# Kernel optimization log

Hardware: AMD Instinct MI355X
Metric: run time of the kernel (lower is better)

## Reference

```python
import jax, jax.numpy as jnp
import numpy as np

H = 2048           # hidden size
IN_F = 64          # in_features
OUT_F = 3          # out_features
NEG_SLOPE = 0.01   # LeakyReLU default


def setup_inputs() -> dict:
    key = jax.random.key(0)
    ks = jax.random.split(key, 11)
    N = 32768
    return {
        "p": jax.random.normal(ks[0], (N, IN_F), dtype=jnp.float32),
        "init_w": jax.random.normal(ks[1], (H, IN_F), dtype=jnp.float32) * 0.05,
        "init_b": jax.random.normal(ks[2], (H,), dtype=jnp.float32) * 0.05,
        "w1": jax.random.normal(ks[3], (H, H), dtype=jnp.float32) * 0.02,
        "b1": jax.random.normal(ks[4], (H,), dtype=jnp.float32) * 0.02,
        "w2": jax.random.normal(ks[5], (H, H), dtype=jnp.float32) * 0.02,
        "b2": jax.random.normal(ks[6], (H,), dtype=jnp.float32) * 0.02,
        "w3": jax.random.normal(ks[7], (H, H), dtype=jnp.float32) * 0.02,
        "b3": jax.random.normal(ks[8], (H,), dtype=jnp.float32) * 0.02,
        "out_w": jax.random.normal(ks[9], (OUT_F, H), dtype=jnp.float32) * 0.05,
        "out_b": jax.random.normal(ks[10], (OUT_F,), dtype=jnp.float32) * 0.05,
    }


def _leaky_relu(x):
    return jnp.where(x > 0, x, NEG_SLOPE * x)


def reference(p, init_w, init_b, w1, b1, w2, b2, w3, b3, out_w, out_b):
    # eval mode: StructuredDropout with eval_size=None -> plain init linear
    flat = p.reshape(-1, p.shape[-1])                      # [N, IN_F]
    x = flat @ init_w.T + init_b                           # [N, H]
    # upper-triangular mask (in==out, backflow=0 -> diagonal=0)
    mask = jnp.triu(jnp.ones((H, H), dtype=bool))
    # hidden TriangleLinear layers; flip = (i % 2 == 1)
    for W, b, flip in ((w1, b1, False), (w2, b2, True), (w3, b3, False)):
        y = _leaky_relu(x) @ jnp.where(mask, W, 0.0).T + b  # [N, H]
        x = y[..., ::-1] if flip else y
    x = _leaky_relu(x)
    out = x @ out_w.T + out_b                              # [N, OUT_F]
    return out.reshape(p.shape[:-1] + (OUT_F,))
```

## Files before the change

kernel.cpp:

```cpp
#include <hip/hip_runtime.h>
#include <hip/hip_bf16.h>

#define NEG 0.01f

using f32x4  = __attribute__((ext_vector_type(4))) float;
using bf16x8 = __attribute__((ext_vector_type(8))) short;

__device__ __forceinline__ unsigned short f2b(float f) {
  union { float f; unsigned int u; } v; v.f = f;
  unsigned int r = (v.u + 0x7fffu + ((v.u >> 16) & 1u)) >> 16;
  return (unsigned short)r;
}
__device__ __forceinline__ float b2f(unsigned int bits) {
  union { unsigned int u; float f; } v; v.u = bits << 16;
  return v.f;
}

__device__ __forceinline__ void gload16(const unsigned short* g, unsigned short* l) {
  __builtin_amdgcn_global_load_lds(
      (const __attribute__((address_space(1))) unsigned int*)g,
      (__attribute__((address_space(3))) unsigned int*)l, 16, 0, 0);
}

__global__ void k_cvt(const float* __restrict__ in, unsigned short* __restrict__ out, int n4) {
  int i = blockIdx.x * blockDim.x + threadIdx.x;
  int stride = gridDim.x * blockDim.x;
  for (; i < n4; i += stride) {
    float4 v = reinterpret_cast<const float4*>(in)[i];
    ushort4 o;
    o.x = f2b(v.x); o.y = f2b(v.y); o.z = f2b(v.z); o.w = f2b(v.w);
    reinterpret_cast<ushort4*>(out)[i] = o;
  }
}

__global__ void k_cvt_tri(const float* __restrict__ W, unsigned short* __restrict__ out, int anti) {
  const int H = 2048;
  int i = blockIdx.x;
  const float* wr = W + (size_t)i * H;
  unsigned short* orow = out + (size_t)i * H;
  if (!anti) {
    for (int j = threadIdx.x; j < H; j += blockDim.x) {
      float v = (j >= i) ? wr[j] : 0.f;
      orow[j] = f2b(v);
    }
  } else {
    for (int k = threadIdx.x; k < H; k += blockDim.x) {
      int j = H - 1 - k;
      float v = (j >= i) ? wr[j] : 0.f;
      orow[k] = f2b(v);
    }
  }
}

__launch_bounds__(512, 2)
__global__ void k_gemm8(const unsigned short* __restrict__ A, int lda,
                        const unsigned short* __restrict__ B, int ldb,
                        const float* __restrict__ bias,
                        unsigned short* __restrict__ C, int ldc,
                        int K, int mode, int NB) {
  extern __shared__ unsigned short lds[];
  const int tid = threadIdx.x;
  const int w   = tid >> 6;
  const int l   = tid & 63;

  const int G = gridDim.x;
  const int P = blockIdx.x;
  const int b = (P & 7) * (G >> 3) + (P >> 3);

  const int srow  = l >> 2;
  const int sperm = ((l & 3) - ((l >> 3) & 3)) & 3;
  const int rdoff = (l & 15) * 64 + ((((l >> 4) + ((l >> 1) & 7)) & 3) << 4);
  const int wm = w >> 2, wn = w & 3;
  const int AbaseW = wm * 16384;
  const int BbaseW = 32768 + (wn >> 1) * 16384 + (wn & 1) * 8192;

  const int npairs = NB * 4;
#pragma unroll 1
  for (int p = b; p < npairs; p += G) {
    const int by = p >> 2;
    const int pr = p & 3;
#pragma unroll 1
    for (int side = 0; side < 2; side++) {
      const int bx = side ? (7 - pr) : pr;
      const int brow = by * 256;
      const int bcol = bx * 256;
      int kstart = 0, kend = K;
      if (mode == 1) kstart = bcol;
      else if (mode == 2) kend = K - bcol;
      const int nt = (kend - kstart) >> 6;

      const unsigned short* Asrc = A + (size_t)(brow + w * 16 + srow) * lda + sperm * 8;
      const unsigned short* Bsrc = B + (size_t)(bcol + w * 16 + srow) * ldb + sperm * 8;

      auto stage_tile = [&](int tk, int bb) {
        const int kc = kstart + (tk << 6);
#pragma unroll
        for (int half = 0; half < 2; half++) {
#pragma unroll
          for (int qq = 0; qq < 2; qq++) {
            gload16(Asrc + (size_t)(half * 128) * lda + kc + qq * 32,
                    (unsigned short*)((char*)lds + bb * 65536 + half * 16384 + (w * 2 + qq) * 1024));
            gload16(Bsrc + (size_t)(half * 128) * ldb + kc + qq * 32,
                    (unsigned short*)((char*)lds + bb * 65536 + 32768 + half * 16384 + (w * 2 + qq) * 1024));
          }
        }
      };

      f32x4 acc[8][4];
#pragma unroll
      for (int i = 0; i < 8; i++)
#pragma unroll
        for (int j = 0; j < 4; j++) acc[i][j] = (f32x4){0.f, 0.f, 0.f, 0.f};

      stage_tile(0, 0);
      if (nt > 1) stage_tile(1, 1);

#pragma unroll 1
      for (int t = 0; t < nt; t++) {
        const int bb = t & 1;
        const char* Ab = (const char*)lds + bb * 65536 + AbaseW;
        const char* Bb = (const char*)lds + bb * 65536 + BbaseW;
        if (t + 1 < nt) asm volatile("s_waitcnt vmcnt(8)" ::: "memory");
        else            asm volatile("s_waitcnt vmcnt(0)" ::: "memory");
        __builtin_amdgcn_s_barrier();
        asm volatile("" ::: "memory");

        bf16x8 a0[4][2], a1[4][2], b0[2][2], b1[2][2];
#pragma unroll
        for (int ii = 0; ii < 4; ii++)
#pragma unroll
          for (int kk = 0; kk < 2; kk++)
            a0[ii][kk] = *(const bf16x8*)(Ab + (ii * 2 + kk) * 1024 + rdoff);
#pragma unroll
        for (int jj = 0; jj < 2; jj++)
#pragma unroll
          for (int kk = 0; kk < 2; kk++)
            b0[jj][kk] = *(const bf16x8*)(Bb + (jj * 2 + kk) * 1024 + rdoff);
        __builtin_amdgcn_s_setprio(1);
#pragma unroll
        for (int ii = 0; ii < 4; ii++)
#pragma unroll
          for (int jj = 0; jj < 2; jj++) {
            acc[ii][jj] = __builtin_amdgcn_mfma_f32_16x16x32_bf16(a0[ii][0], b0[jj][0], acc[ii][jj], 0, 0, 0);
            acc[ii][jj] = __builtin_amdgcn_mfma_f32_16x16x32_bf16(a0[ii][1], b0[jj][1], acc[ii][jj], 0, 0, 0);
          }
        __builtin_amdgcn_s_setprio(0);
#pragma unroll
        for (int jj = 0; jj < 2; jj++)
#pragma unroll
          for (int kk = 0; kk < 2; kk++)
            b1[jj][kk] = *(const bf16x8*)(Bb + ((2 + jj) * 2 + kk) * 1024 + rdoff);
        __builtin_amdgcn_s_setprio(1);
#pragma unroll
        for (int ii = 0; ii < 4; ii++)
#pragma unroll
          for (int jj = 0; jj < 2; jj++) {
            acc[ii][2 + jj] = __builtin_amdgcn_mfma_f32_16x16x32_bf16(a0[ii][0], b1[jj][0], acc[ii][2 + jj], 0, 0, 0);
            acc[ii][2 + jj] = __builtin_amdgcn_mfma_f32_16x16x32_bf16(a0[ii][1], b1[jj][1], acc[ii][2 + jj], 0, 0, 0);
          }
        __builtin_amdgcn_s_setprio(0);
#pragma unroll
        for (int ii = 0; ii < 4; ii++)
#pragma unroll
          for (int kk = 0; kk < 2; kk++)
            a1[ii][kk] = *(const bf16x8*)(Ab + ((4 + ii) * 2 + kk) * 1024 + rdoff);
        __builtin_amdgcn_s_setprio(1);
#pragma unroll
        for (int ii = 0; ii < 4; ii++)
#pragma unroll
          for (int jj = 0; jj < 2; jj++) {
            acc[4 + ii][2 + jj] = __builtin_amdgcn_mfma_f32_16x16x32_bf16(a1[ii][0], b1[jj][0], acc[4 + ii][2 + jj], 0, 0, 0);
            acc[4 + ii][2 + jj] = __builtin_amdgcn_mfma_f32_16x16x32_bf16(a1[ii][1], b1[jj][1], acc[4 + ii][2 + jj], 0, 0, 0);
          }
        __builtin_amdgcn_s_setprio(0);
        __builtin_amdgcn_s_setprio(1);
#pragma unroll
        for (int ii = 0; ii < 4; ii++)
#pragma unroll
          for (int jj = 0; jj < 2; jj++) {
            acc[4 + ii][jj] = __builtin_amdgcn_mfma_f32_16x16x32_bf16(a1[ii][0], b0[jj][0], acc[4 + ii][jj], 0, 0, 0);
            acc[4 + ii][jj] = __builtin_amdgcn_mfma_f32_16x16x32_bf16(a1[ii][1], b0[jj][1], acc[4 + ii][jj], 0, 0, 0);
          }
        __builtin_amdgcn_s_setprio(0);

        asm volatile("s_waitcnt lgkmcnt(0)" ::: "memory");
        __builtin_amdgcn_s_barrier();
        asm volatile("" ::: "memory");
        if (t + 2 < nt) stage_tile(t + 2, bb);
      }

      const int orow0 = brow + wm * 128 + ((l >> 4) << 2);
      const int ocol0 = bcol + wn * 64 + (l & 15);
#pragma unroll
      for (int j = 0; j < 4; j++) {
        const int col = ocol0 + j * 16;
        const float bv = bias[col];
#pragma unroll
        for (int i = 0; i < 8; i++) {
#pragma unroll
          for (int r = 0; r < 4; r++) {
            const int row = orow0 + i * 16 + r;
            float v = acc[i][j][r] + bv;
            v = v > 0.f ? v : NEG * v;
            C[(size_t)row * ldc + col] = f2b(v);
          }
        }
      }
    }
  }
}

__global__ void k_out(const unsigned short* __restrict__ A,
                      const float* __restrict__ ow, const float* __restrict__ ob,
                      float* __restrict__ out) {
  const int H = 2048;
  int w = threadIdx.x >> 6, lane = threadIdx.x & 63;
  size_t n = (size_t)blockIdx.x * 4 + w;
  const unsigned short* a = A + n * H;
  float s0 = 0.f, s1 = 0.f, s2 = 0.f;
  for (int h0 = lane * 8; h0 < H; h0 += 512) {
    uint4 u = *reinterpret_cast<const uint4*>(&a[h0]);
    unsigned int uu[4] = {u.x, u.y, u.z, u.w};
#pragma unroll
    for (int q = 0; q < 4; q++) {
      int h = h0 + q * 2;
      float x0 = b2f(uu[q] & 0xffffu);
      float x1 = b2f(uu[q] >> 16);
      s0 += x0 * ow[h]         + x1 * ow[h + 1];
      s1 += x0 * ow[H + h]     + x1 * ow[H + h + 1];
      s2 += x0 * ow[2 * H + h] + x1 * ow[2 * H + h + 1];
    }
  }
#pragma unroll
  for (int off = 32; off > 0; off >>= 1) {
    s0 += __shfl_down(s0, off);
    s1 += __shfl_down(s1, off);
    s2 += __shfl_down(s2, off);
  }
  if (lane == 0) {
    out[n * 3 + 0] = s0 + ob[0];
    out[n * 3 + 1] = s1 + ob[1];
    out[n * 3 + 2] = s2 + ob[2];
  }
}

extern "C" void kernel_launch(void* const* d_in, const int* in_sizes, int n_in,
                              void* d_out, int out_size, void* d_ws, size_t ws_size,
                              hipStream_t stream) {
  const int N = 32768, H = 2048, INF_ = 64;
  const float* p      = (const float*)d_in[0];
  const float* init_w = (const float*)d_in[1];
  const float* init_b = (const float*)d_in[2];
  const float* w1     = (const float*)d_in[3];
  const float* b1     = (const float*)d_in[4];
  const float* w2     = (const float*)d_in[5];
  const float* b2     = (const float*)d_in[6];
  const float* w3     = (const float*)d_in[7];
  const float* b3     = (const float*)d_in[8];
  const float* ow     = (const float*)d_in[9];
  const float* ob     = (const float*)d_in[10];

  hipFuncSetAttribute((const void*)k_gemm8,
                      hipFuncAttributeMaxDynamicSharedMemorySize, 131072);

  char* wsb = (char*)d_ws;
  size_t off = 0;
  auto alloc = [&](size_t bytes) -> char* {
    char* q = wsb + off;
    off += (bytes + 255) & ~(size_t)255;
    return q;
  };
  unsigned short* pb  = (unsigned short*)alloc((size_t)N * INF_ * 2);
  unsigned short* iwb = (unsigned short*)alloc((size_t)H * INF_ * 2);
  unsigned short* w1m = (unsigned short*)alloc((size_t)H * H * 2);
  unsigned short* w2m = (unsigned short*)alloc((size_t)H * H * 2);
  unsigned short* w3m = (unsigned short*)alloc((size_t)H * H * 2);

  size_t remain = (ws_size > off) ? (ws_size - off) : 0;
  long long ncll = (long long)(remain / ((size_t)H * 2 * 2));
  int Nc = (int)((ncll / 256) * 256);
  if (Nc > N) Nc = N;
  if (Nc < 256) return;

  unsigned short* bufA = (unsigned short*)(wsb + off);
  unsigned short* bufB = bufA + (size_t)Nc * H;

  k_cvt<<<2048, 256, 0, stream>>>(p, pb, N * INF_ / 4);
  k_cvt<<<32,   256, 0, stream>>>(init_w, iwb, H * INF_ / 4);
  k_cvt_tri<<<H, 256, 0, stream>>>(w1, w1m, 0);
  k_cvt_tri<<<H, 256, 0, stream>>>(w2, w2m, 0);
  k_cvt_tri<<<H, 256, 0, stream>>>(w3, w3m, 1);

  for (int n0 = 0; n0 < N; n0 += Nc) {
    int nc = (N - n0 < Nc) ? (N - n0) : Nc;
    int NB = nc / 256;
    k_gemm8<<<256, 512, 131072, stream>>>(pb + (size_t)n0 * INF_, INF_, iwb, INF_,
                                          init_b, bufA, H, INF_, 0, NB);
    k_gemm8<<<256, 512, 131072, stream>>>(bufA, H, w1m, H, b1, bufB, H, H, 1, NB);
    k_gemm8<<<256, 512, 131072, stream>>>(bufB, H, w2m, H, b2, bufA, H, H, 1, NB);
    k_gemm8<<<256, 512, 131072, stream>>>(bufA, H, w3m, H, b3, bufB, H, H, 2, NB);
    k_out<<<nc / 4, 256, 0, stream>>>(bufB, ow, ob, (float*)d_out + (size_t)n0 * 3);
  }
}
```

Before: 972.4 us.

## Restructure GEMM to 16-wave blocks with 32-wide K tiles and static LDS

The GEMM kernel moves from 512 to 1024 threads per block. The 256x256 block tile is now split across 16 waves, each computing a 64x64 sub-tile instead of 128x64. The K step shrinks from 64 to 32, so double-buffered LDS fits in 64KB of static shared memory, and the grid doubles to 512 blocks. The aim is more resident waves for latency hiding and less register pressure from a smaller accumulator. In exchange there are twice as many barriers per K, and each wave gets less reuse from every fragment it reads out of LDS.

Result: slower. 1.235 ms (+27.0%).

```diff
diff --git a/kernel.cpp b/kernel.cpp
--- a/kernel.cpp
+++ b/kernel.cpp
@@ -52,13 +52,13 @@
   }
 }
 
-__launch_bounds__(512, 2)
+__launch_bounds__(1024, 2)
 __global__ void k_gemm8(const unsigned short* __restrict__ A, int lda,
                         const unsigned short* __restrict__ B, int ldb,
                         const float* __restrict__ bias,
                         unsigned short* __restrict__ C, int ldc,
                         int K, int mode, int NB) {
-  extern __shared__ unsigned short lds[];
+  __shared__ unsigned short lds[32768];
   const int tid = threadIdx.x;
   const int w   = tid >> 6;
   const int l   = tid & 63;
@@ -71,8 +71,6 @@
   const int sperm = ((l & 3) - ((l >> 3) & 3)) & 3;
   const int rdoff = (l & 15) * 64 + ((((l >> 4) + ((l >> 1) & 7)) & 3) << 4);
   const int wm = w >> 2, wn = w & 3;
-  const int AbaseW = wm * 16384;
-  const int BbaseW = 32768 + (wn >> 1) * 16384 + (wn & 1) * 8192;
 
   const int npairs = NB * 4;
 #pragma unroll 1
@@ -87,28 +85,20 @@
       int kstart = 0, kend = K;
       if (mode == 1) kstart = bcol;
       else if (mode == 2) kend = K - bcol;
-      const int nt = (kend - kstart) >> 6;
+      const int nt = (kend - kstart) >> 5;
 
       const unsigned short* Asrc = A + (size_t)(brow + w * 16 + srow) * lda + sperm * 8;
       const unsigned short* Bsrc = B + (size_t)(bcol + w * 16 + srow) * ldb + sperm * 8;
 
       auto stage_tile = [&](int tk, int bb) {
-        const int kc = kstart + (tk << 6);
-#pragma unroll
-        for (int half = 0; half < 2; half++) {
-#pragma unroll
-          for (int qq = 0; qq < 2; qq++) {
-            gload16(Asrc + (size_t)(half * 128) * lda + kc + qq * 32,
-                    (unsigned short*)((char*)lds + bb * 65536 + half * 16384 + (w * 2 + qq) * 1024));
-            gload16(Bsrc + (size_t)(half * 128) * ldb + kc + qq * 32,
-                    (unsigned short*)((char*)lds + bb * 65536 + 32768 + half * 16384 + (w * 2 + qq) * 1024));
-          }
-        }
+        const int kc = kstart + (tk << 5);
+        gload16(Asrc + kc, (unsigned short*)((char*)lds + bb * 32768 + w * 1024));
+        gload16(Bsrc + kc, (unsigned short*)((char*)lds + bb * 32768 + 16384 + w * 1024));
       };
 
-      f32x4 acc[8][4];
-#pragma unroll
-      for (int i = 0; i < 8; i++)
+      f32x4 acc[4][4];
+#pragma unroll
+      for (int i = 0; i < 4; i++)
 #pragma unroll
         for (int j = 0; j < 4; j++) acc[i][j] = (f32x4){0.f, 0.f, 0.f, 0.f};
 
@@ -118,69 +108,26 @@
 #pragma unroll 1
       for (int t = 0; t < nt; t++) {
         const int bb = t & 1;
-        const char* Ab = (const char*)lds + bb * 65536 + AbaseW;
-        const char* Bb = (const char*)lds + bb * 65536 + BbaseW;
-        if (t + 1 < nt) asm volatile("s_waitcnt vmcnt(8)" ::: "memory");
+        const char* Ab = (const char*)lds + bb * 32768;
+        const char* Bb = (const char*)lds + bb * 32768 + 16384;
+        if (t + 1 < nt) asm volatile("s_waitcnt vmcnt(2)" ::: "memory");
         else            asm volatile("s_waitcnt vmcnt(0)" ::: "memory");
         __builtin_amdgcn_s_barrier();
         asm volatile("" ::: "memory");
 
-        bf16x8 a0[4][2], a1[4][2], b0[2][2], b1[2][2];
-#pragma unroll
-        for (int ii = 0; ii < 4; ii++)
-#pragma unroll
-          for (int kk = 0; kk < 2; kk++)
-            a0[ii][kk] = *(const bf16x8*)(Ab + (ii * 2 + kk) * 1024 + rdoff);
-#pragma unroll
-        for (int jj = 0; jj < 2; jj++)
-#pragma unroll
-          for (int kk = 0; kk < 2; kk++)
-            b0[jj][kk] = *(const bf16x8*)(Bb + (jj * 2 + kk) * 1024 + rdoff);
+        bf16x8 af[4], bfr[4];
+#pragma unroll
+        for (int i = 0; i < 4; i++)
+          af[i] = *(const bf16x8*)(Ab + (wm * 4 + i) * 1024 + rdoff);
+#pragma unroll
+        for (int j = 0; j < 4; j++)
+          bfr[j] = *(const bf16x8*)(Bb + (wn * 4 + j) * 1024 + rdoff);
         __builtin_amdgcn_s_setprio(1);
 #pragma unroll
-        for (int ii = 0; ii < 4; ii++)
-#pragma unroll
-          for (int jj = 0; jj < 2; jj++) {
-            acc[ii][jj] = __builtin_amdgcn_mfma_f32_16x16x32_bf16(a0[ii][0], b0[jj][0], acc[ii][jj], 0, 0, 0);
-            acc[ii][jj] = __builtin_amdgcn_mfma_f32_16x16x32_bf16(a0[ii][1], b0[jj][1], acc[ii][jj], 0, 0, 0);
-          }
-        __builtin_amdgcn_s_setprio(0);
-#pragma unroll
-        for (int jj = 0; jj < 2; jj++)
-#pragma unroll
-          for (int kk = 0; kk < 2; kk++)
-            b1[jj][kk] = *(const bf16x8*)(Bb + ((2 + jj) * 2 + kk) * 1024 + rdoff);
-        __builtin_amdgcn_s_setprio(1);
-#pragma unroll
-        for (int ii = 0; ii < 4; ii++)
-#pragma unroll
-          for (int jj = 0; jj < 2; jj++) {
-            acc[ii][2 + jj] = __builtin_amdgcn_mfma_f32_16x16x32_bf16(a0[ii][0], b1[jj][0], acc[ii][2 + jj], 0, 0, 0);
-            acc[ii][2 + jj] = __builtin_amdgcn_mfma_f32_16x16x32_bf16(a0[ii][1], b1[jj][1], acc[ii][2 + jj], 0, 0, 0);
-          }
-        __builtin_amdgcn_s_setprio(0);
-#pragma unroll
-        for (int ii = 0; ii < 4; ii++)
-#pragma unroll
-          for (int kk = 0; kk < 2; kk++)
-            a1[ii][kk] = *(const bf16x8*)(Ab + ((4 + ii) * 2 + kk) * 1024 + rdoff);
-        __builtin_amdgcn_s_setprio(1);
-#pragma unroll
-        for (int ii = 0; ii < 4; ii++)
-#pragma unroll
-          for (int jj = 0; jj < 2; jj++) {
-            acc[4 + ii][2 + jj] = __builtin_amdgcn_mfma_f32_16x16x32_bf16(a1[ii][0], b1[jj][0], acc[4 + ii][2 + jj], 0, 0, 0);
-            acc[4 + ii][2 + jj] = __builtin_amdgcn_mfma_f32_16x16x32_bf16(a1[ii][1], b1[jj][1], acc[4 + ii][2 + jj], 0, 0, 0);
-          }
-        __builtin_amdgcn_s_setprio(0);
-        __builtin_amdgcn_s_setprio(1);
-#pragma unroll
-        for (int ii = 0; ii < 4; ii++)
-#pragma unroll
-          for (int jj = 0; jj < 2; jj++) {
-            acc[4 + ii][jj] = __builtin_amdgcn_mfma_f32_16x16x32_bf16(a1[ii][0], b0[jj][0], acc[4 + ii][jj], 0, 0, 0);
-            acc[4 + ii][jj] = __builtin_amdgcn_mfma_f32_16x16x32_bf16(a1[ii][1], b0[jj][1], acc[4 + ii][jj], 0, 0, 0);
-          }
+        for (int i = 0; i < 4; i++)
+#pragma unroll
+          for (int j = 0; j < 4; j++)
+            acc[i][j] = __builtin_amdgcn_mfma_f32_16x16x32_bf16(af[i], bfr[j], acc[i][j], 0, 0, 0);
         __builtin_amdgcn_s_setprio(0);
 
         asm volatile("s_waitcnt lgkmcnt(0)" ::: "memory");
@@ -189,14 +136,14 @@
         if (t + 2 < nt) stage_tile(t + 2, bb);
       }
 
-      const int orow0 = brow + wm * 128 + ((l >> 4) << 2);
+      const int orow0 = brow + wm * 64 + ((l >> 4) << 2);
       const int ocol0 = bcol + wn * 64 + (l & 15);
 #pragma unroll
       for (int j = 0; j < 4; j++) {
         const int col = ocol0 + j * 16;
         const float bv = bias[col];
 #pragma unroll
-        for (int i = 0; i < 8; i++) {
+        for (int i = 0; i < 4; i++) {
 #pragma unroll
           for (int r = 0; r < 4; r++) {
             const int row = orow0 + i * 16 + r;
@@ -260,9 +207,6 @@
   const float* ow     = (const float*)d_in[9];
   const float* ob     = (const float*)d_in[10];
 
-  hipFuncSetAttribute((const void*)k_gemm8,
-                      hipFuncAttributeMaxDynamicSharedMemorySize, 131072);
-
   char* wsb = (char*)d_ws;
   size_t off = 0;
   auto alloc = [&](size_t bytes) -> char* {
@@ -294,11 +238,11 @@
   for (int n0 = 0; n0 < N; n0 += Nc) {
     int nc = (N - n0 < Nc) ? (N - n0) : Nc;
     int NB = nc / 256;
-    k_gemm8<<<256, 512, 131072, stream>>>(pb + (size_t)n0 * INF_, INF_, iwb, INF_,
-                                          init_b, bufA, H, INF_, 0, NB);
-    k_gemm8<<<256, 512, 131072, stream>>>(bufA, H, w1m, H, b1, bufB, H, H, 1, NB);
-    k_gemm8<<<256, 512, 131072, stream>>>(bufB, H, w2m, H, b2, bufA, H, H, 1, NB);
-    k_gemm8<<<256, 512, 131072, stream>>>(bufA, H, w3m, H, b3, bufB, H, H, 2, NB);
+    k_gemm8<<<512, 1024, 0, stream>>>(pb + (size_t)n0 * INF_, INF_, iwb, INF_,
+                                      init_b, bufA, H, INF_, 0, NB);
+    k_gemm8<<<512, 1024, 0, stream>>>(bufA, H, w1m, H, b1, bufB, H, H, 1, NB);
+    k_gemm8<<<512, 1024, 0, stream>>>(bufB, H, w2m, H, b2, bufA, H, H, 1, NB);
+    k_gemm8<<<512, 1024, 0, stream>>>(bufA, H, w3m, H, b3, bufB, H, H, 2, NB);
     k_out<<<nc / 4, 256, 0, stream>>>(bufB, ow, ob, (float*)d_out + (size_t)n0 * 3);
   }
 }
```
